# Optimization experiments

Hardware: AMD Instinct MI355X
Metric: run time of the kernel (lower is better)

## Reference

```python
import jax, jax.numpy as jnp
import numpy as np

LN_EPS = 1e-5
NEG = -1e9


def _layernorm(x, g, b):
    m = jnp.mean(x, axis=-1, keepdims=True)
    v = jnp.mean(jnp.square(x - m), axis=-1, keepdims=True)
    return (x - m) * jax.lax.rsqrt(v + LN_EPS) * g + b


def setup_inputs() -> dict:
    key = jax.random.key(0)
    ks = jax.random.split(key, 16)
    B, S, E, H, D = 4, 2048, 1024, 16, 64
    s = 0.02
    return {
        "x": jax.random.normal(ks[0], (B, S, E), jnp.float32),
        "mask": jax.random.randint(ks[1], (B, S), 0, 2, jnp.int32),
        "Wq": jax.random.normal(ks[2], (H, E, D), jnp.float32) * s,
        "bq": jnp.zeros((H, D), jnp.float32),
        "Wk": jax.random.normal(ks[3], (H, E, D), jnp.float32) * s,
        "bk": jnp.zeros((H, D), jnp.float32),
        "Wv": jax.random.normal(ks[4], (H, E, D), jnp.float32) * s,
        "bv": jnp.zeros((H, D), jnp.float32),
        "Wo": jax.random.normal(ks[5], (H * D, E), jnp.float32) * s,
        "bo": jnp.zeros((E,), jnp.float32),
        "g1": jnp.ones((E,), jnp.float32),
        "b1": jnp.zeros((E,), jnp.float32),
        "W1": jax.random.normal(ks[6], (E, D), jnp.float32) * s,
        "c1": jnp.zeros((D,), jnp.float32),
        "W2": jax.random.normal(ks[7], (D, E), jnp.float32) * s,
        "c2": jnp.zeros((E,), jnp.float32),
        "g2": jnp.ones((E,), jnp.float32),
        "b2": jnp.zeros((E,), jnp.float32),
    }


def reference(x, mask, Wq, bq, Wk, bk, Wv, bv, Wo, bo, g1, b1, W1, c1, W2, c2, g2, b2):
    B, S, E = x.shape
    # per-head projections, batched over heads: [B,H,S,D]
    q = jnp.einsum('bse,hed->bhsd', x, Wq) + bq[None, :, None, :]
    k = jnp.einsum('bse,hed->bhsd', x, Wk) + bk[None, :, None, :]
    v = jnp.einsum('bse,hed->bhsd', x, Wv) + bv[None, :, None, :]
    # NOTE: original scales by sqrt(seq_len) (query.size(1)), not sqrt(head_dim)
    scale = jnp.asarray(S, x.dtype) ** 0.5
    scores = jnp.einsum('bhsd,bhtd->bhst', q, k) / scale
    scores = jnp.where(mask[:, None, None, :] == 0, NEG, scores)
    attn = jax.nn.softmax(scores, axis=-1)
    ctx = jnp.einsum('bhst,bhtd->bhsd', attn, v)
    # concat heads: [B,S,H*D]
    ctx = ctx.transpose(0, 2, 1, 3).reshape(B, S, -1)
    h = _layernorm(ctx @ Wo + bo, g1, b1)
    # bottleneck FFN (dropout = identity at eval), exact GELU
    f = jax.nn.gelu(h @ W1 + c1, approximate=False) @ W2 + c2
    # no residual connection in the original module
    return _layernorm(f, g2, b2)
```

## Files before the change

kernel.cpp:

```cpp
#include <hip/hip_runtime.h>
#include <math.h>

#define B_ 4
#define S_ 2048
#define E_ 1024
#define H_ 16
#define D_ 64
#define M_ (B_*S_)
#define QSCALE (0.022097086912079608f * 1.4426950408889634f)

typedef __bf16 bf16_t;
typedef __bf16 bf16x8 __attribute__((ext_vector_type(8)));
typedef float  f32x4  __attribute__((ext_vector_type(4)));

__device__ __forceinline__ void gload_lds16(const void* g, void* l) {
    __builtin_amdgcn_global_load_lds(
        (const __attribute__((address_space(1))) void*)g,
        (__attribute__((address_space(3))) void*)l, 16, 0, 0);
}
__device__ __forceinline__ bf16x8 ldsx8(const void* p) {
    return __builtin_bit_cast(bf16x8, *(const uint4*)p);
}
__device__ __forceinline__ unsigned short bf16bits(float x) {
    return __builtin_bit_cast(unsigned short, (bf16_t)x);
}
template<int N> __device__ __forceinline__ void waitv() {
    if constexpr (N == 4) asm volatile("s_waitcnt vmcnt(4) lgkmcnt(0)" ::: "memory");
    else                  asm volatile("s_waitcnt vmcnt(0) lgkmcnt(0)" ::: "memory");
}
__device__ __forceinline__ int fk(int row) { return ((row & 3) + 2 * ((row >> 3) & 3)) & 7; }

template<int BM, int BN, int MODE>
__global__ __launch_bounds__(256) void gemm_bf16(
    const bf16_t* __restrict__ A, const bf16_t* __restrict__ Bt,
    bf16_t* __restrict__ ob0, bf16_t* __restrict__ ob1, bf16_t* __restrict__ ob2,
    const float* __restrict__ bias0, const float* __restrict__ bias1,
    const int* __restrict__ sidx, const int* __restrict__ nkv,
    int M, int N, int K)
{
    constexpr int FM = BM / 32, FN = BN / 32;
    __shared__ bf16_t As[BM * 64];
    __shared__ bf16_t Bs[BN * 64];

    const int tid = threadIdx.x;
    const int w   = tid >> 6;
    const int wr  = w >> 1, wc = w & 1;
    const int lr  = tid & 15;
    const int lg  = (tid >> 4) & 3;

    const int nwg  = gridDim.x * gridDim.y;
    int bidf = blockIdx.y * gridDim.x + blockIdx.x;
    bidf = (bidf & 7) * (nwg >> 3) + (bidf >> 3);
    const int bm = (bidf / gridDim.x) * BM;
    const int bn = (bidf % gridDim.x) * BN;

    int arow[FM];
    if constexpr (MODE == 2) {
        const int b2 = bm >> 11, rbase = bm & 2047;
        const int nkp128 = (nkv[b2] + 127) & ~127;
        if (rbase >= nkp128) return;
        #pragma unroll
        for (int i = 0; i < FM; ++i) {
            const int row = (i * 256 + tid) >> 3;
            arow[i] = (b2 << 11) + sidx[(b2 << 11) + rbase + row];
        }
    }

    f32x4 acc[FM][FN] = {};

    for (int kk = 0; kk < K; kk += 64) {
        __syncthreads();
        #pragma unroll
        for (int i = 0; i < BM / 32; ++i) {
            int idx = i * 256 + tid;
            int row = idx >> 3, slot = idx & 7;
            const size_t grow = (MODE == 2) ? (size_t)arow[i] : (size_t)(bm + row);
            gload_lds16(A + grow * K + kk + (slot ^ (row & 7)) * 8,
                        (char*)As + idx * 16);
        }
        #pragma unroll
        for (int i = 0; i < BN / 32; ++i) {
            int idx = i * 256 + tid;
            int row = idx >> 3, slot = idx & 7;
            gload_lds16(Bt + (size_t)(bn + row) * K + kk + (slot ^ (row & 7)) * 8,
                        (char*)Bs + idx * 16);
        }
        __syncthreads();

        #pragma unroll
        for (int h = 0; h < 2; ++h) {
            bf16x8 af[FM], bfr[FN];
            #pragma unroll
            for (int m = 0; m < FM; ++m) {
                int row = wr * (BM / 2) + m * 16 + lr;
                af[m] = ldsx8((char*)As + row * 128 + (((4 * h + lg) ^ (row & 7)) << 4));
            }
            #pragma unroll
            for (int n = 0; n < FN; ++n) {
                int col = wc * (BN / 2) + n * 16 + lr;
                bfr[n] = ldsx8((char*)Bs + col * 128 + (((4 * h + lg) ^ (col & 7)) << 4));
            }
            #pragma unroll
            for (int m = 0; m < FM; ++m)
                #pragma unroll
                for (int n = 0; n < FN; ++n)
                    acc[m][n] = __builtin_amdgcn_mfma_f32_16x16x32_bf16(
                        af[m], bfr[n], acc[m][n], 0, 0, 0);
        }
    }

    #pragma unroll
    for (int n = 0; n < FN; ++n) {
        const int gcol = bn + wc * (BN / 2) + n * 16 + lr;
        if constexpr (MODE == 2) {
            const int p = gcol >> 10, nn = gcol & 1023;
            const int b2 = bm >> 11;
            const float bvl = p ? bias1[nn] : bias0[nn];
            #pragma unroll
            for (int m = 0; m < FM; ++m) {
                const int ci0 = (bm & 2047) + wr * (BM / 2) + m * 16 + lg * 4;
                if (p) {
                    ushort4 o;
                    o.x = bf16bits(acc[m][n][0] + bvl);
                    o.y = bf16bits(acc[m][n][1] + bvl);
                    o.z = bf16bits(acc[m][n][2] + bvl);
                    o.w = bf16bits(acc[m][n][3] + bvl);
                    *(ushort4*)(ob2 + ((((size_t)b2 << 10) + nn) << 11) + ci0) = o;
                } else {
                    #pragma unroll
                    for (int r = 0; r < 4; ++r)
                        ob1[((size_t)((b2 << 11) + ci0 + r) << 10) + nn] =
                            (bf16_t)(acc[m][n][r] + bvl);
                }
            }
        } else {
            const float bvl = bias0[gcol];
            #pragma unroll
            for (int m = 0; m < FM; ++m)
                #pragma unroll
                for (int r = 0; r < 4; ++r) {
                    const int grow = bm + wr * (BM / 2) + m * 16 + lg * 4 + r;
                    float v = acc[m][n][r] + bvl;
                    if constexpr (MODE == 1)
                        v = 0.5f * v * (1.0f + erff(v * 0.70710678118654752f));
                    ob0[(size_t)grow * N + gcol] = (bf16_t)v;
                }
        }
    }
}

__global__ __launch_bounds__(256) void compact_mask(
    const int* __restrict__ mask, int* __restrict__ sidx, int* __restrict__ nkv)
{
    __shared__ int wsum[4];
    const int b = blockIdx.x;
    const int tid = threadIdx.x;
    const int lane = tid & 63, wv = tid >> 6;
    const int base = tid * 8;

    int m[8], loc[8];
    int cnt = 0;
    #pragma unroll
    for (int j = 0; j < 8; ++j) {
        m[j] = mask[b * S_ + base + j];
        loc[j] = cnt;
        cnt += (m[j] != 0);
    }
    int incl = cnt;
    #pragma unroll
    for (int off = 1; off < 64; off <<= 1) {
        int t = __shfl_up(incl, off);
        if (lane >= off) incl += t;
    }
    if (lane == 63) wsum[wv] = incl;
    const int excl_lane = incl - cnt;
    __syncthreads();
    int wbase = 0;
    for (int i = 0; i < wv; ++i) wbase += wsum[i];
    const int total = wsum[0] + wsum[1] + wsum[2] + wsum[3];
    if (tid == 0) nkv[b] = total;
    const int tbase = wbase + excl_lane;
    #pragma unroll
    for (int j = 0; j < 8; ++j)
        if (m[j]) sidx[b * S_ + tbase + loc[j]] = base + j;

    const int nkp = (total + 127) & ~127;
    for (int c = total + tid; c < nkp; c += 256)
        sidx[b * S_ + c] = 0;
}

__global__ __launch_bounds__(256) void attn_mfma(
    const bf16_t* __restrict__ qg, const bf16_t* __restrict__ kg,
    const bf16_t* __restrict__ vg, const int* __restrict__ nkv,
    bf16_t* __restrict__ ctx)
{
    __shared__ bf16_t ks[2][64 * 64];
    __shared__ bf16_t vts[2][64 * 64];

    const int tid = threadIdx.x;
    const int w   = tid >> 6;
    const int lr  = tid & 15;
    const int lg  = (tid >> 4) & 3;

    const int bid = blockIdx.x;
    const int xcd = bid & 7, kidx = bid >> 3;
    const int bh  = xcd * 8 + (kidx >> 4);
    const int xq  = kidx & 15;
    const int b   = bh >> 4, h = bh & 15;
    const int q0w = xq * 128 + w * 32;

    const int nk = nkv[b];
    const int ntiles = (nk + 63) >> 6;
    const bool hastail = (nk & 63) != 0;

    bf16x8 aq[2][2];
    #pragma unroll
    for (int f = 0; f < 2; ++f) {
        const bf16_t* qp = qg + ((size_t)(b * S_ + q0w + f * 16 + lr) << 10) + h * 64 + lg * 8;
        aq[f][0] = ldsx8(qp);
        aq[f][1] = ldsx8(qp + 32);
    }

    bf16x8 onesf;
    {
        bf16_t o1 = (bf16_t)((lr == 0) ? 1.0f : 0.0f);
        #pragma unroll
        for (int j = 0; j < 8; ++j) onesf[j] = o1;
    }

    int koff[2][2][2], voff[2][4];
    #pragma unroll
    for (int c = 0; c < 2; ++c) {
        #pragma unroll
        for (int kf1 = 0; kf1 < 2; ++kf1) {
            const int row = c * 32 + 8 * (lr >> 2) + 4 * kf1 + (lr & 3);
            const int f = fk(row);
            koff[c][kf1][0] = row * 128 + ((lg ^ f) << 4);
            koff[c][kf1][1] = row * 128 + (((4 + lg) ^ f) << 4);
        }
        #pragma unroll
        for (int n = 0; n < 4; ++n) {
            const int rowv = n * 16 + lr;
            voff[c][n] = rowv * 128 + (((4 * c + lg) ^ (rowv & 7)) << 4);
        }
    }

    const bf16_t* kptr[2];
    const bf16_t* vptr[2];
    char* kdst[2];
    char* vdst[2];
    #pragma unroll
    for (int it = 0; it < 2; ++it) {
        const int idx = it * 256 + tid;
        const int row = idx >> 3, slot = idx & 7;
        kptr[it] = kg + ((size_t)((b << 11) + row) << 10) + h * 64 + (slot ^ fk(row)) * 8;
        vptr[it] = vg + (((size_t)bh * 64 + row) << 11) + (slot ^ (row & 7)) * 8;
        kdst[it] = (char*)ks + idx * 16;
        vdst[it] = (char*)vts + idx * 16;
    }

    f32x4 accO[2][4] = {};
    f32x4 accL[2] = {};

    auto STAGE = [&](int buf) {
        const int nb = buf << 13;
        #pragma unroll
        for (int it = 0; it < 2; ++it) {
            gload_lds16(kptr[it], kdst[it] + nb);
            gload_lds16(vptr[it], vdst[it] + nb);
            kptr[it] += (size_t)64 << 10;
            vptr[it] += 64;
        }
    };

    auto COMPUTE = [&](int buf, int t0, bool tl) {
        const char* ksb = (const char*)ks + (buf << 13);
        const char* vsb = (const char*)vts + (buf << 13);
        #pragma unroll
        for (int c = 0; c < 2; ++c) {
            unsigned int pw0[4], pw1[4];
            #pragma unroll
            for (int kf1 = 0; kf1 < 2; ++kf1) {
                bf16x8 a0 = ldsx8(ksb + koff[c][kf1][0]);
                bf16x8 a1 = ldsx8(ksb + koff[c][kf1][1]);
                f32x4 z0 = {}, z1 = {};
                if (tl) {
                    const int keyb = t0 + c * 32 + 8 * lg + 4 * kf1;
                    f32x4 bias;
                    #pragma unroll
                    for (int r = 0; r < 4; ++r)
                        bias[r] = (keyb + r < nk) ? 0.0f : -1.0e9f;
                    z0 = bias; z1 = bias;
                }
                __builtin_amdgcn_s_setprio(1);
                z0 = __builtin_amdgcn_mfma_f32_16x16x32_bf16(a0, aq[0][0], z0, 0, 0, 0);
                z0 = __builtin_amdgcn_mfma_f32_16x16x32_bf16(a1, aq[0][1], z0, 0, 0, 0);
                z1 = __builtin_amdgcn_mfma_f32_16x16x32_bf16(a0, aq[1][0], z1, 0, 0, 0);
                z1 = __builtin_amdgcn_mfma_f32_16x16x32_bf16(a1, aq[1][1], z1, 0, 0, 0);
                __builtin_amdgcn_s_setprio(0);
                const float p00 = __builtin_amdgcn_exp2f(z0[0]);
                const float p01 = __builtin_amdgcn_exp2f(z0[1]);
                const float p02 = __builtin_amdgcn_exp2f(z0[2]);
                const float p03 = __builtin_amdgcn_exp2f(z0[3]);
                const float p10 = __builtin_amdgcn_exp2f(z1[0]);
                const float p11 = __builtin_amdgcn_exp2f(z1[1]);
                const float p12 = __builtin_amdgcn_exp2f(z1[2]);
                const float p13 = __builtin_amdgcn_exp2f(z1[3]);
                pw0[2 * kf1]     = bf16bits(p00) | ((unsigned)bf16bits(p01) << 16);
                pw0[2 * kf1 + 1] = bf16bits(p02) | ((unsigned)bf16bits(p03) << 16);
                pw1[2 * kf1]     = bf16bits(p10) | ((unsigned)bf16bits(p11) << 16);
                pw1[2 * kf1 + 1] = bf16bits(p12) | ((unsigned)bf16bits(p13) << 16);
            }
            uint4 pk0 = {pw0[0], pw0[1], pw0[2], pw0[3]};
            uint4 pk1 = {pw1[0], pw1[1], pw1[2], pw1[3]};
            const bf16x8 pa0 = __builtin_bit_cast(bf16x8, pk0);
            const bf16x8 pa1 = __builtin_bit_cast(bf16x8, pk1);

            __builtin_amdgcn_s_setprio(1);
            #pragma unroll
            for (int n = 0; n < 4; ++n) {
                bf16x8 av = ldsx8(vsb + voff[c][n]);
                accO[0][n] = __builtin_amdgcn_mfma_f32_16x16x32_bf16(av, pa0, accO[0][n], 0, 0, 0);
                accO[1][n] = __builtin_amdgcn_mfma_f32_16x16x32_bf16(av, pa1, accO[1][n], 0, 0, 0);
            }
            accL[0] = __builtin_amdgcn_mfma_f32_16x16x32_bf16(onesf, pa0, accL[0], 0, 0, 0);
            accL[1] = __builtin_amdgcn_mfma_f32_16x16x32_bf16(onesf, pa1, accL[1], 0, 0, 0);
            __builtin_amdgcn_s_setprio(0);
        }
    };

    STAGE(0);
    int cur = 0;
    for (int t = 0; t < ntiles; ++t) {
        if (t + 1 < ntiles) {
            STAGE(cur ^ 1);
            waitv<4>();
        } else {
            waitv<0>();
        }
        __builtin_amdgcn_s_barrier();
        COMPUTE(cur, t * 64, hastail && (t == ntiles - 1));
        __builtin_amdgcn_s_barrier();
        cur ^= 1;
    }

    #pragma unroll
    for (int f = 0; f < 2; ++f) {
        const float inv = 1.0f / __shfl(accL[f][0], lr);
        bf16_t* obase = ctx + ((size_t)(b * S_ + q0w + f * 16 + lr) << 10) + h * 64;
        #pragma unroll
        for (int n = 0; n < 4; ++n) {
            ushort4 o;
            o.x = bf16bits(accO[f][n][0] * inv);
            o.y = bf16bits(accO[f][n][1] * inv);
            o.z = bf16bits(accO[f][n][2] * inv);
            o.w = bf16bits(accO[f][n][3] * inv);
            *(ushort4*)(obase + n * 16 + lg * 4) = o;
        }
    }
}

__global__ __launch_bounds__(256) void prep_all(
    const float* __restrict__ x, bf16_t* __restrict__ xb,
    const float* __restrict__ Wq, const float* __restrict__ Wk,
    const float* __restrict__ Wv, bf16_t* __restrict__ WqkvT,
    const float* __restrict__ Wo, bf16_t* __restrict__ WoT,
    const float* __restrict__ W1, bf16_t* __restrict__ W1T,
    const float* __restrict__ W2, bf16_t* __restrict__ W2T,
    const float* __restrict__ bq, float* __restrict__ bqs)
{
    __shared__ float t[32][33];
    const int tid = threadIdx.x;
    int bid = blockIdx.x;

    if (bid < 4096) {
        int i = bid * 256 + tid;
        float4 a = ((const float4*)x)[i * 2];
        float4 b = ((const float4*)x)[i * 2 + 1];
        unsigned int p0 = bf16bits(a.x) | ((unsigned)bf16bits(a.y) << 16);
        unsigned int p1 = bf16bits(a.z) | ((unsigned)bf16bits(a.w) << 16);
        unsigned int p2 = bf16bits(b.x) | ((unsigned)bf16bits(b.y) << 16);
        unsigned int p3 = bf16bits(b.z) | ((unsigned)bf16bits(b.w) << 16);
        uint4 o = {p0, p1, p2, p3};
        ((uint4*)xb)[i] = o;
        return;
    }
    bid -= 4096;

    if (bid == 4224) {
        #pragma unroll
        for (int j = 0; j < 4; ++j)
            bqs[tid * 4 + j] = bq[tid * 4 + j] * QSCALE;
        return;
    }

    const float* in; bf16_t* out;
    int R, C, c0, r0;
    float scale = 1.0f;
    if (bid < 3072) {
        const int p = bid >> 10, r = bid & 1023;
        const int z = r >> 6, rem = r & 63;
        in  = (p == 0 ? Wq : p == 1 ? Wk : Wv) + z * 65536;
        out = WqkvT + p * 1048576 + z * 65536;
        R = 1024; C = 64;
        c0 = (rem & 1) * 32; r0 = (rem >> 1) * 32;
        if (p == 0) scale = QSCALE;
    } else if (bid < 4096) {
        const int r = bid - 3072;
        in = Wo; out = WoT; R = 1024; C = 1024;
        c0 = (r & 31) * 32; r0 = (r >> 5) * 32;
    } else if (bid < 4160) {
        const int r = bid - 4096;
        in = W1; out = W1T; R = 1024; C = 64;
        c0 = (r & 1) * 32; r0 = (r >> 1) * 32;
    } else {
        const int r = bid - 4160;
        in = W2; out = W2T; R = 64; C = 1024;
        c0 = (r & 31) * 32; r0 = (r >> 5) * 32;
    }

    {
        int rr = tid >> 3, c4 = (tid & 7) * 4;
        float4 v = *(const float4*)&in[(size_t)(r0 + rr) * C + c0 + c4];
        t[rr][c4 + 0] = v.x * scale;
        t[rr][c4 + 1] = v.y * scale;
        t[rr][c4 + 2] = v.z * scale;
        t[rr][c4 + 3] = v.w * scale;
    }
    __syncthreads();
    {
        int c = tid >> 3, r4 = (tid & 7) * 4;
        ushort4 o;
        o.x = bf16bits(t[r4 + 0][c]);
        o.y = bf16bits(t[r4 + 1][c]);
        o.z = bf16bits(t[r4 + 2][c]);
        o.w = bf16bits(t[r4 + 3][c]);
        *(ushort4*)(out + (size_t)(c0 + c) * R + r0 + r4) = o;
    }
}

template<typename InT, typename OutT>
__global__ __launch_bounds__(256) void ln_kernel(
    const InT* __restrict__ in, const float* __restrict__ g,
    const float* __restrict__ bta, OutT* __restrict__ out)
{
    const int row = blockIdx.x;
    const int tid = threadIdx.x;

    float x0, x1, x2, x3;
    if constexpr (sizeof(InT) == 4) {
        float4 xv = ((const float4*)(in + (size_t)row * E_))[tid];
        x0 = xv.x; x1 = xv.y; x2 = xv.z; x3 = xv.w;
    } else {
        ushort4 xv = *(const ushort4*)((const bf16_t*)in + (size_t)row * E_ + tid * 4);
        x0 = (float)__builtin_bit_cast(bf16_t, xv.x);
        x1 = (float)__builtin_bit_cast(bf16_t, xv.y);
        x2 = (float)__builtin_bit_cast(bf16_t, xv.z);
        x3 = (float)__builtin_bit_cast(bf16_t, xv.w);
    }
    float s  = x0 + x1 + x2 + x3;
    float sq = x0 * x0 + x1 * x1 + x2 * x2 + x3 * x3;
    #pragma unroll
    for (int off = 32; off > 0; off >>= 1) {
        s  += __shfl_down(s, off);
        sq += __shfl_down(sq, off);
    }
    __shared__ float ss[4], ssq[4];
    if ((tid & 63) == 0) { ss[tid >> 6] = s; ssq[tid >> 6] = sq; }
    __syncthreads();
    s  = ss[0] + ss[1] + ss[2] + ss[3];
    sq = ssq[0] + ssq[1] + ssq[2] + ssq[3];

    const float mean = s * (1.0f / E_);
    const float var  = sq * (1.0f / E_) - mean * mean;
    const float rstd = rsqrtf(var + 1e-5f);

    float4 gv = ((const float4*)g)[tid];
    float4 bv = ((const float4*)bta)[tid];
    float o0 = (x0 - mean) * rstd * gv.x + bv.x;
    float o1 = (x1 - mean) * rstd * gv.y + bv.y;
    float o2 = (x2 - mean) * rstd * gv.z + bv.z;
    float o3 = (x3 - mean) * rstd * gv.w + bv.w;
    if constexpr (sizeof(OutT) == 4) {
        float4 o = {o0, o1, o2, o3};
        ((float4*)((float*)out + (size_t)row * E_))[tid] = o;
    } else {
        ushort4 o;
        o.x = bf16bits(o0); o.y = bf16bits(o1);
        o.z = bf16bits(o2); o.w = bf16bits(o3);
        *(ushort4*)((bf16_t*)out + (size_t)row * E_ + tid * 4) = o;
    }
}

extern "C" void kernel_launch(void* const* d_in, const int* in_sizes, int n_in,
                              void* d_out, int out_size, void* d_ws, size_t ws_size,
                              hipStream_t stream)
{
    const float* x    = (const float*)d_in[0];
    const int*   mask = (const int*)d_in[1];
    const float* Wq   = (const float*)d_in[2];
    const float* bq   = (const float*)d_in[3];
    const float* Wk   = (const float*)d_in[4];
    const float* bk   = (const float*)d_in[5];
    const float* Wv   = (const float*)d_in[6];
    const float* bv   = (const float*)d_in[7];
    const float* Wo   = (const float*)d_in[8];
    const float* bo   = (const float*)d_in[9];
    const float* g1   = (const float*)d_in[10];
    const float* b1   = (const float*)d_in[11];
    const float* W1   = (const float*)d_in[12];
    const float* c1   = (const float*)d_in[13];
    const float* W2   = (const float*)d_in[14];
    const float* c2   = (const float*)d_in[15];
    const float* g2   = (const float*)d_in[16];
    const float* b2   = (const float*)d_in[17];

    char* W = (char*)d_ws;
    bf16_t* xb    = (bf16_t*)(W + 0);
    bf16_t* WqkvT = (bf16_t*)(W + 16777216);
    bf16_t* WoT   = (bf16_t*)(W + 23068672);
    bf16_t* W1T   = (bf16_t*)(W + 25165824);
    bf16_t* W2T   = (bf16_t*)(W + 25296896);
    bf16_t* qbuf  = (bf16_t*)(W + 25427968);
    bf16_t* kbuf  = (bf16_t*)(W + 42205184);
    bf16_t* vtc   = (bf16_t*)(W + 58982400);
    bf16_t* ctx   = (bf16_t*)(W + 75759616);
    bf16_t* t1b   = (bf16_t*)(W + 25427968);
    bf16_t* hb    = (bf16_t*)(W + 42205184);
    bf16_t* f1b   = (bf16_t*)(W + 0);
    bf16_t* f2b   = (bf16_t*)(W + 58982400);
    int*    sidx  = (int*)(W + 92536832);
    int*    nkv   = (int*)(W + 92569600);
    float*  bqs   = (float*)(W + 92569664);
    float*  out   = (float*)d_out;

    prep_all<<<8321, 256, 0, stream>>>(x, xb, Wq, Wk, Wv, WqkvT,
                                       Wo, WoT, W1, W1T, W2, W2T, bq, bqs);

    compact_mask<<<4, 256, 0, stream>>>(mask, sidx, nkv);

    gemm_bf16<128, 128, 0><<<dim3(8, 64), 256, 0, stream>>>(
        xb, WqkvT, qbuf, nullptr, nullptr, bqs, nullptr, nullptr, nullptr,
        M_, 1024, 1024);

    gemm_bf16<128, 128, 2><<<dim3(16, 64), 256, 0, stream>>>(
        xb, WqkvT + (1 << 20), nullptr, kbuf, vtc, bk, bv, sidx, nkv,
        M_, 2048, 1024);

    attn_mfma<<<dim3(1024), 256, 0, stream>>>(qbuf, kbuf, vtc, nkv, ctx);

    gemm_bf16<128, 128, 0><<<dim3(8, 64), 256, 0, stream>>>(
        ctx, WoT, t1b, nullptr, nullptr, bo, nullptr, nullptr, nullptr,
        M_, 1024, 1024);

    ln_kernel<bf16_t, bf16_t><<<8192, 256, 0, stream>>>(t1b, g1, b1, hb);

    gemm_bf16<32, 64, 1><<<dim3(1, 256), 256, 0, stream>>>(
        hb, W1T, f1b, nullptr, nullptr, c1, nullptr, nullptr, nullptr,
        M_, 64, 1024);

    gemm_bf16<128, 128, 0><<<dim3(8, 64), 256, 0, stream>>>(
        f1b, W2T, f2b, nullptr, nullptr, c2, nullptr, nullptr, nullptr,
        M_, 1024, 64);

    ln_kernel<bf16_t, float><<<8192, 256, 0, stream>>>(f2b, g2, b2, out);
}
```

Baseline: 209.7 us.

## Double-buffer GEMM LDS tiles to overlap global loads with MFMA

Turns the bf16 GEMM main loop into a two-stage pipeline with two LDS buffers for each operand. The next K-tile is issued with global_load_lds before computing on the current one, and a partial vmcnt wait lets the in-flight loads continue. The goal is to hide global-memory latency behind MFMA work instead of stalling at a barrier each iteration. In exchange LDS use per block doubles, which can lower occupancy, and tile shapes whose load count has no matching wait case fall back to waiting on all loads, which removes the overlap for those shapes.

After: 201.8 us. -3.8%, faster.

```diff
diff --git a/kernel.cpp b/kernel.cpp
--- a/kernel.cpp
+++ b/kernel.cpp
@@ -25,8 +25,10 @@
     return __builtin_bit_cast(unsigned short, (bf16_t)x);
 }
 template<int N> __device__ __forceinline__ void waitv() {
-    if constexpr (N == 4) asm volatile("s_waitcnt vmcnt(4) lgkmcnt(0)" ::: "memory");
-    else                  asm volatile("s_waitcnt vmcnt(0) lgkmcnt(0)" ::: "memory");
+    if constexpr (N == 8)      asm volatile("s_waitcnt vmcnt(8) lgkmcnt(0)" ::: "memory");
+    else if constexpr (N == 4) asm volatile("s_waitcnt vmcnt(4) lgkmcnt(0)" ::: "memory");
+    else if constexpr (N == 3) asm volatile("s_waitcnt vmcnt(3) lgkmcnt(0)" ::: "memory");
+    else                       asm volatile("s_waitcnt vmcnt(0) lgkmcnt(0)" ::: "memory");
 }
 __device__ __forceinline__ int fk(int row) { return ((row & 3) + 2 * ((row >> 3) & 3)) & 7; }
 
@@ -39,8 +41,9 @@
     int M, int N, int K)
 {
     constexpr int FM = BM / 32, FN = BN / 32;
-    __shared__ bf16_t As[BM * 64];
-    __shared__ bf16_t Bs[BN * 64];
+    constexpr int NL = BM / 32 + BN / 32;
+    __shared__ bf16_t As[2][BM * 64];
+    __shared__ bf16_t Bs[2][BN * 64];
 
     const int tid = threadIdx.x;
     const int w   = tid >> 6;
@@ -64,41 +67,44 @@
             const int row = (i * 256 + tid) >> 3;
             arow[i] = (b2 << 11) + sidx[(b2 << 11) + rbase + row];
         }
+    } else {
+        #pragma unroll
+        for (int i = 0; i < FM; ++i)
+            arow[i] = bm + ((i * 256 + tid) >> 3);
     }
 
     f32x4 acc[FM][FN] = {};
 
-    for (int kk = 0; kk < K; kk += 64) {
-        __syncthreads();
+    auto STAGE = [&](int buf, int kk) {
         #pragma unroll
         for (int i = 0; i < BM / 32; ++i) {
             int idx = i * 256 + tid;
             int row = idx >> 3, slot = idx & 7;
-            const size_t grow = (MODE == 2) ? (size_t)arow[i] : (size_t)(bm + row);
-            gload_lds16(A + grow * K + kk + (slot ^ (row & 7)) * 8,
-                        (char*)As + idx * 16);
+            gload_lds16(A + (size_t)arow[i] * K + kk + (slot ^ (row & 7)) * 8,
+                        (char*)As[buf] + idx * 16);
         }
         #pragma unroll
         for (int i = 0; i < BN / 32; ++i) {
             int idx = i * 256 + tid;
             int row = idx >> 3, slot = idx & 7;
             gload_lds16(Bt + (size_t)(bn + row) * K + kk + (slot ^ (row & 7)) * 8,
-                        (char*)Bs + idx * 16);
-        }
-        __syncthreads();
-
+                        (char*)Bs[buf] + idx * 16);
+        }
+    };
+
+    auto COMPUTE = [&](int buf) {
         #pragma unroll
         for (int h = 0; h < 2; ++h) {
             bf16x8 af[FM], bfr[FN];
             #pragma unroll
             for (int m = 0; m < FM; ++m) {
                 int row = wr * (BM / 2) + m * 16 + lr;
-                af[m] = ldsx8((char*)As + row * 128 + (((4 * h + lg) ^ (row & 7)) << 4));
+                af[m] = ldsx8((char*)As[buf] + row * 128 + (((4 * h + lg) ^ (row & 7)) << 4));
             }
             #pragma unroll
             for (int n = 0; n < FN; ++n) {
                 int col = wc * (BN / 2) + n * 16 + lr;
-                bfr[n] = ldsx8((char*)Bs + col * 128 + (((4 * h + lg) ^ (col & 7)) << 4));
+                bfr[n] = ldsx8((char*)Bs[buf] + col * 128 + (((4 * h + lg) ^ (col & 7)) << 4));
             }
             #pragma unroll
             for (int m = 0; m < FM; ++m)
@@ -107,6 +113,21 @@
                     acc[m][n] = __builtin_amdgcn_mfma_f32_16x16x32_bf16(
                         af[m], bfr[n], acc[m][n], 0, 0, 0);
         }
+    };
+
+    STAGE(0, 0);
+    int cur = 0;
+    for (int kk = 0; kk < K; kk += 64) {
+        if (kk + 64 < K) {
+            STAGE(cur ^ 1, kk + 64);
+            waitv<NL>();
+        } else {
+            waitv<0>();
+        }
+        __builtin_amdgcn_s_barrier();
+        COMPUTE(cur);
+        __builtin_amdgcn_s_barrier();
+        cur ^= 1;
     }
 
     #pragma unroll
```
